# Kernel optimization log

Hardware: AMD Instinct MI355X
Metric: run time of the kernel (lower is better)

The kernel has to match this reference:

```python
import jax, jax.numpy as jnp
import numpy as np

N_NODES = 100000
NEG_SLOPE = 0.2  # PyG GATConv default


def gat_conv(x, W, att_src, att_dst, bias, src, dst, heads, out_ch, concat):
    """PyG-style GATConv (eval mode, self-loops already appended to src/dst).

    x: [N, F_in]; W: [F_in, heads*out_ch]; att_src/att_dst: [heads, out_ch];
    bias: [heads*out_ch] if concat else [out_ch].
    """
    n = x.shape[0]
    h = (x @ W).reshape(n, heads, out_ch)               # [N, H, C]
    a_s = jnp.einsum('nhc,hc->nh', h, att_src)          # [N, H]
    a_d = jnp.einsum('nhc,hc->nh', h, att_dst)          # [N, H]
    e = jax.nn.leaky_relu(a_s[src] + a_d[dst], NEG_SLOPE)  # [E, H]
    # segment softmax over incoming edges of each destination node
    m = jax.ops.segment_max(e, dst, num_segments=n)     # [N, H]
    ex = jnp.exp(e - m[dst])                            # [E, H]
    denom = jax.ops.segment_sum(ex, dst, num_segments=n)
    alpha = ex / denom[dst]                             # [E, H]
    msg = h[src] * alpha[:, :, None]                    # [E, H, C]
    out = jax.ops.segment_sum(msg, dst, num_segments=n) # [N, H, C]
    if concat:
        out = out.reshape(n, heads * out_ch)
    else:
        out = out.mean(axis=1)
    return out + bias


def setup_inputs() -> dict:
    key = jax.random.key(0)
    ks = jax.random.split(key, 12)
    N, F_IN, H1, C1, NC = N_NODES, 32, 8, 8, 2
    E = 3200000
    x = jax.random.normal(ks[0], (N, F_IN), dtype=jnp.float32)
    edge_index = jax.random.randint(ks[1], (2, E), 0, N, dtype=jnp.int64)
    s = 0.3
    return {
        'x': x,
        'edge_index': edge_index,
        'W1': jax.random.normal(ks[2], (F_IN, H1 * C1), dtype=jnp.float32) * s,
        'att_src1': jax.random.normal(ks[3], (H1, C1), dtype=jnp.float32) * s,
        'att_dst1': jax.random.normal(ks[4], (H1, C1), dtype=jnp.float32) * s,
        'b1': jnp.zeros((H1 * C1,), dtype=jnp.float32),
        'W2': jax.random.normal(ks[5], (H1 * C1, NC), dtype=jnp.float32) * s,
        'att_src2': jax.random.normal(ks[6], (1, NC), dtype=jnp.float32) * s,
        'att_dst2': jax.random.normal(ks[7], (1, NC), dtype=jnp.float32) * s,
        'b2': jnp.zeros((NC,), dtype=jnp.float32),
    }


def reference(x, W1, att_src1, att_dst1, b1, W2, att_src2, att_dst2, b2, edge_index):
    n = x.shape[0]
    # PyG GATConv adds self-loops by default
    loops = jnp.arange(n, dtype=edge_index.dtype)
    src = jnp.concatenate([edge_index[0], loops])
    dst = jnp.concatenate([edge_index[1], loops])
    # eval mode: all dropouts are identity
    h = jax.nn.elu(gat_conv(x, W1, att_src1, att_dst1, b1, src, dst, 8, 8, True))
    out = gat_conv(h, W2, att_src2, att_dst2, b2, src, dst, 1, 2, True)
    return jax.nn.log_softmax(out, axis=1)
```

## Files before the change

kernel.cpp:

```cpp
#include <hip/hip_runtime.h>
#include <math.h>

#define F_IN 32
#define NH 8
#define C1 8
#define D1 64
#define NEG 0.2f
#define LOG2E 1.44269504088896f
#define SHBIAS (-20.0f * LOG2E)

typedef int iv4 __attribute__((ext_vector_type(4)));
typedef unsigned short ushort_t;

__device__ __forceinline__ ushort_t f2bf(float f) {
    unsigned int b = __float_as_uint(f);
    return (ushort_t)((b + 0x7FFF + ((b >> 16) & 1)) >> 16);
}
__device__ __forceinline__ float bf2f(ushort_t u) {
    return __uint_as_float(((unsigned int)u) << 16);
}


__device__ __forceinline__ void node1_body(const float* __restrict__ x, const float* __restrict__ W1,
                                           const float* __restrict__ as1, const float* __restrict__ ad1,
                                           ushort_t* __restrict__ h1b, float* __restrict__ a_s,
                                           float* __restrict__ a_d, int N, int b) {
    __shared__ float sW[F_IN * D1];
    __shared__ float sA[2 * D1];
    for (int i = threadIdx.x; i < F_IN * D1; i += blockDim.x) sW[i] = W1[i];
    if (threadIdx.x < 2 * D1)
        sA[threadIdx.x] = (threadIdx.x < D1) ? as1[threadIdx.x] : ad1[threadIdx.x - D1];
    __syncthreads();
    int t = b * blockDim.x + threadIdx.x;
    int n = t >> 3, h = t & 7;
    if (n >= N) return;
    float xr[F_IN];
    const float4* xv = (const float4*)(x + n * F_IN);
#pragma unroll
    for (int k = 0; k < F_IN / 4; ++k) {
        float4 v = xv[k];
        xr[4 * k] = v.x; xr[4 * k + 1] = v.y; xr[4 * k + 2] = v.z; xr[4 * k + 3] = v.w;
    }
    float acc[C1];
#pragma unroll
    for (int c = 0; c < C1; ++c) acc[c] = 0.0f;
#pragma unroll
    for (int k = 0; k < F_IN; ++k) {
        float xk = xr[k];
#pragma unroll
        for (int c = 0; c < C1; ++c) acc[c] = fmaf(xk, sW[k * D1 + h * C1 + c], acc[c]);
    }
    float s_ = 0.0f, d_ = 0.0f;
    unsigned int w[4];
#pragma unroll
    for (int c = 0; c < C1; ++c) {
        s_ = fmaf(acc[c], sA[h * C1 + c], s_);
        d_ = fmaf(acc[c], sA[D1 + h * C1 + c], d_);
    }
#pragma unroll
    for (int k = 0; k < 4; ++k)
        w[k] = (unsigned int)f2bf(acc[2 * k]) | ((unsigned int)f2bf(acc[2 * k + 1]) << 16);
    iv4 wv = {(int)w[0], (int)w[1], (int)w[2], (int)w[3]};
    *(iv4*)(h1b + (size_t)n * D1 + h * C1) = wv;
    a_s[n * NH + h] = s_;
    a_d[n * NH + h] = d_;
}

__global__ void __launch_bounds__(256)
k_bhist_node1(const int* __restrict__ ei, int E4, int GA, int nbk,
              int* __restrict__ blkcnt,
              const float* __restrict__ x, const float* __restrict__ W1,
              const float* __restrict__ as1, const float* __restrict__ ad1,
              ushort_t* __restrict__ h1b, float* __restrict__ a_s, float* __restrict__ a_d,
              int N) {
    int g = blockIdx.x;
    if (g >= GA) { node1_body(x, W1, as1, ad1, h1b, a_s, a_d, N, g - GA); return; }
    __shared__ int hist[512];
    for (int i = threadIdx.x; i < nbk; i += 256) hist[i] = 0;
    __syncthreads();
    const iv4* d4 = (const iv4*)ei + E4;
    int base = g * 2048 + threadIdx.x;
#pragma unroll
    for (int k = 0; k < 8; ++k) {
        int idx = base + k * 256;
        if (idx < E4) {
            iv4 d = __builtin_nontemporal_load(d4 + idx);
            atomicAdd(&hist[d.x >> 8], 1);
            atomicAdd(&hist[d.y >> 8], 1);
            atomicAdd(&hist[d.z >> 8], 1);
            atomicAdd(&hist[d.w >> 8], 1);
        }
    }
    __syncthreads();
    for (int i = threadIdx.x; i < nbk; i += 256) blkcnt[(size_t)i * GA + g] = hist[i];
}

__global__ void k_scan_block(const int* __restrict__ in, int* __restrict__ tmp,
                             int* __restrict__ bsum, int F) {
    __shared__ int s[256];
    int i = blockIdx.x * 256 + threadIdx.x;
    int v = (i < F) ? in[i] : 0;
    s[threadIdx.x] = v;
    __syncthreads();
#pragma unroll
    for (int off = 1; off < 256; off <<= 1) {
        int t = (threadIdx.x >= off) ? s[threadIdx.x - off] : 0;
        __syncthreads();
        s[threadIdx.x] += t;
        __syncthreads();
    }
    tmp[i] = s[threadIdx.x] - v;
    if (threadIdx.x == 255) bsum[blockIdx.x] = s[255];
}

__global__ void k_scan_bsums1024(int* __restrict__ bsum, int nb) {
    __shared__ int s[1024];
    int t = threadIdx.x;
    s[t] = (t < nb) ? bsum[t] : 0;
    __syncthreads();
#pragma unroll
    for (int off = 1; off < 1024; off <<= 1) {
        int v = (t >= off) ? s[t - off] : 0;
        __syncthreads();
        s[t] += v;
        __syncthreads();
    }
    if (t < nb) bsum[t] = (t == 0) ? 0 : s[t - 1];
}

__global__ void k_scan_fin(const int* __restrict__ tmp, const int* __restrict__ bsum,
                           int* __restrict__ excl, int F, int E) {
    int i = blockIdx.x * blockDim.x + threadIdx.x;
    if (i > F) return;
    excl[i] = (i < F) ? (tmp[i] + bsum[i >> 8]) : E;
}

__global__ void __launch_bounds__(256)
k_part(const int* __restrict__ ei, int E4, int GA, int nbk,
       const int* __restrict__ excl, int* __restrict__ partbuf) {
    __shared__ int cur[512];
    int g = blockIdx.x;
    for (int i = threadIdx.x; i < nbk; i += 256) cur[i] = excl[(size_t)i * GA + g];
    __syncthreads();
    const iv4* s4 = (const iv4*)ei;
    const iv4* d4 = s4 + E4;
    int base = g * 2048 + threadIdx.x;
#pragma unroll
    for (int k = 0; k < 8; ++k) {
        int idx = base + k * 256;
        if (idx < E4) {
            iv4 d = __builtin_nontemporal_load(d4 + idx);
            iv4 s = __builtin_nontemporal_load(s4 + idx);
            int dd[4] = {d.x, d.y, d.z, d.w};
            int ss[4] = {s.x, s.y, s.z, s.w};
#pragma unroll
            for (int u = 0; u < 4; ++u) {
                int pos = atomicAdd(&cur[dd[u] >> 8], 1);
                partbuf[pos] = (ss[u] << 8) | (dd[u] & 255);
            }
        }
    }
}

__global__ void __launch_bounds__(256)
k_csr(const int* __restrict__ excl, const int* __restrict__ partbuf,
      int* __restrict__ ptr, int* __restrict__ srcs, int N, int GA, int nbk, int Et) {
    __shared__ int lcnt[256];
    __shared__ int lsc[256];
    int b = blockIdx.x;
    int tid = threadIdx.x;
    int pStart = excl[(size_t)b * GA];
    int pEnd   = excl[(size_t)(b + 1) * GA];
    int node = (b << 8) + tid;
    int exists = (node < N) ? 1 : 0;
    lcnt[tid] = exists;
    __syncthreads();
    for (int i = pStart + tid; i < pEnd; i += 256)
        atomicAdd(&lcnt[partbuf[i] & 255], 1);
    __syncthreads();
    int v = lcnt[tid];
    lsc[tid] = v;
    __syncthreads();
#pragma unroll
    for (int off = 1; off < 256; off <<= 1) {
        int t = (tid >= off) ? lsc[tid - off] : 0;
        __syncthreads();
        lsc[tid] += t;
        __syncthreads();
    }
    int exclv = lsc[tid] - v;
    int finalBase = pStart + (b << 8);
    if (exists) {
        int p = finalBase + exclv;
        ptr[node] = p;
        srcs[p] = node;
    }
    if (b == nbk - 1 && tid == 0) ptr[N] = Et;
    __syncthreads();
    lcnt[tid] = exclv + exists;
    __syncthreads();
    for (int i = pStart + tid; i < pEnd; i += 256) {
        int pv = partbuf[i];
        int r = atomicAdd(&lcnt[pv & 255], 1);
        srcs[finalBase + r] = pv >> 8;
    }
}


__device__ __forceinline__ float lrelu(float e) { return e > 0.0f ? e : NEG * e; }

__global__ void __launch_bounds__(256)
k_gat1(const int* __restrict__ ptr, const int* __restrict__ srcs,
       const float* __restrict__ a_s, const float* __restrict__ a_d,
       const ushort_t* __restrict__ h1b,
       const float* __restrict__ b1, const float* __restrict__ W2,
       const float* __restrict__ as2, const float* __restrict__ ad2,
       float* __restrict__ h2, float* __restrict__ a_s2o, float* __restrict__ a_d2o,
       int N) {
    int n = (blockIdx.x * blockDim.x + threadIdx.x) >> 6;
    if (n >= N) return;
    int l = threadIdx.x & 63;
    int j = l >> 3;
    int h = l & 7;
    int start = ptr[n], end = ptr[n + 1];
    float ad = a_d[n * NH + h];
    const ushort_t* hb = h1b + l;
    float den = 0.0f, acc = 0.0f;
    for (int base = start; base < end; base += 8) {
        int idxl = base + j;
        bool valid = idxl < end;
        if (!valid) idxl = end - 1;
        int s = srcs[idxl];
        float as = a_s[(s << 3) + h];
        float ex = exp2f(fmaf(lrelu(as + ad), LOG2E, SHBIAS));
        if (!valid) ex = 0.0f;
        den += ex;
        int s0 = __builtin_amdgcn_readlane(s, 0),  s1 = __builtin_amdgcn_readlane(s, 8);
        int s2 = __builtin_amdgcn_readlane(s, 16), s3 = __builtin_amdgcn_readlane(s, 24);
        int s4 = __builtin_amdgcn_readlane(s, 32), s5 = __builtin_amdgcn_readlane(s, 40);
        int s6 = __builtin_amdgcn_readlane(s, 48), s7 = __builtin_amdgcn_readlane(s, 56);
        float g0 = bf2f(hb[s0 << 6]), g1 = bf2f(hb[s1 << 6]);
        float g2 = bf2f(hb[s2 << 6]), g3 = bf2f(hb[s3 << 6]);
        float g4 = bf2f(hb[s4 << 6]), g5 = bf2f(hb[s5 << 6]);
        float g6 = bf2f(hb[s6 << 6]), g7 = bf2f(hb[s7 << 6]);
        int bl = l >> 3;
        float e0 = __shfl(ex, 0 + bl, 64),  e1 = __shfl(ex, 8 + bl, 64);
        float e2 = __shfl(ex, 16 + bl, 64), e3 = __shfl(ex, 24 + bl, 64);
        float e4 = __shfl(ex, 32 + bl, 64), e5 = __shfl(ex, 40 + bl, 64);
        float e6 = __shfl(ex, 48 + bl, 64), e7 = __shfl(ex, 56 + bl, 64);
        acc = fmaf(e0, g0, acc); acc = fmaf(e1, g1, acc);
        acc = fmaf(e2, g2, acc); acc = fmaf(e3, g3, acc);
        acc = fmaf(e4, g4, acc); acc = fmaf(e5, g5, acc);
        acc = fmaf(e6, g6, acc); acc = fmaf(e7, g7, acc);
    }
    den += __shfl_xor(den, 8, 64);
    den += __shfl_xor(den, 16, 64);
    den += __shfl_xor(den, 32, 64);
    den = __shfl(den, l >> 3, 64);
    float v = acc / den + b1[l];
    v = v > 0.0f ? v : expm1f(v);
    float r0 = v * W2[l * 2 + 0];
    float r1 = v * W2[l * 2 + 1];
#pragma unroll
    for (int off = 32; off; off >>= 1) {
        r0 += __shfl_xor(r0, off, 64);
        r1 += __shfl_xor(r1, off, 64);
    }
    if (l == 0) {
        h2[n * 2 + 0] = r0;
        h2[n * 2 + 1] = r1;
        a_s2o[n] = r0 * as2[0] + r1 * as2[1];
        a_d2o[n] = r0 * ad2[0] + r1 * ad2[1];
    }
}


__global__ void k_gat2(const int* __restrict__ ptr, const int* __restrict__ srcs,
                       const float* __restrict__ a_s2, const float* __restrict__ a_d2,
                       const float* __restrict__ h2, const float* __restrict__ b2,
                       float* __restrict__ out, int N) {
    int t = blockIdx.x * blockDim.x + threadIdx.x;
    int n = t >> 4;
    if (n >= N) return;
    int l = threadIdx.x & 15;
    int start = ptr[n], end = ptr[n + 1];
    float ad = a_d2[n];
    float den = 0.0f, a0 = 0.0f, a1 = 0.0f;
    for (int idx = start + l; idx < end; idx += 16) {
        int s = srcs[idx];
        float ex = exp2f(fmaf(lrelu(a_s2[s] + ad), LOG2E, SHBIAS));
        float2 hv = *(const float2*)(h2 + s * 2);
        den += ex;
        a0 = fmaf(ex, hv.x, a0);
        a1 = fmaf(ex, hv.y, a1);
    }
#pragma unroll
    for (int off = 8; off; off >>= 1) {
        den += __shfl_xor(den, off, 16);
        a0  += __shfl_xor(a0, off, 16);
        a1  += __shfl_xor(a1, off, 16);
    }
    if (l == 0) {
        float inv = 1.0f / den;
        float o0 = a0 * inv + b2[0];
        float o1 = a1 * inv + b2[1];
        float mx = fmaxf(o0, o1);
        float lse = mx + logf(__expf(o0 - mx) + __expf(o1 - mx));
        out[n * 2 + 0] = o0 - lse;
        out[n * 2 + 1] = o1 - lse;
    }
}

extern "C" void kernel_launch(void* const* d_in, const int* in_sizes, int n_in,
                              void* d_out, int out_size, void* d_ws, size_t ws_size,
                              hipStream_t stream) {
    const float* x   = (const float*)d_in[0];
    const int*   ei  = (const int*)d_in[1];
    const float* W1  = (const float*)d_in[2];
    const float* as1 = (const float*)d_in[3];
    const float* ad1 = (const float*)d_in[4];
    const float* b1  = (const float*)d_in[5];
    const float* W2  = (const float*)d_in[6];
    const float* as2 = (const float*)d_in[7];
    const float* ad2 = (const float*)d_in[8];
    const float* b2  = (const float*)d_in[9];
    float* out = (float*)d_out;

    const int N  = in_sizes[0] / F_IN;
    const int E  = in_sizes[1] / 2;
    const int E4 = E / 4;
    const int Et = E + N;
    const int nbk = (N + 255) >> 8;
    const int GA  = (E4 + 2047) >> 11;
    const int F   = nbk * GA;
    const int nbScan = (F + 255) >> 8;

    char* p = (char*)d_ws;
    ushort_t* h1b = (ushort_t*)p; p += (size_t)N * D1 * 2;
    float* a_s1 = (float*)p; p += (size_t)N * NH * 4;
    float* a_d1 = (float*)p; p += (size_t)N * NH * 4;
    float* h2   = (float*)p; p += (size_t)N * 2 * 4;
    float* a_s2 = (float*)p; p += (size_t)N * 4;
    float* a_d2 = (float*)p; p += (size_t)N * 4;
    int* blkcnt = (int*)p;   p += (size_t)F * 4;
    int* tmp    = (int*)p;   p += (size_t)nbScan * 256 * 4;
    int* bsum   = (int*)p;   p += (size_t)nbScan * 4;
    int* excl   = (int*)p;   p += (size_t)(F + 1) * 4;
    int* partbuf= (int*)p;   p += (size_t)E * 4;
    int* ptr    = (int*)p;   p += (size_t)(N + 1) * 4;
    int* srcs   = (int*)p;   p += (size_t)Et * 4;

    const int nN1 = (N * NH + 255) / 256;

    hipLaunchKernelGGL(k_bhist_node1, dim3(GA + nN1), dim3(256), 0, stream,
                       ei, E4, GA, nbk, blkcnt, x, W1, as1, ad1, h1b, a_s1, a_d1, N);

    hipLaunchKernelGGL(k_scan_block, dim3(nbScan), dim3(256), 0, stream, blkcnt, tmp, bsum, F);
    hipLaunchKernelGGL(k_scan_bsums1024, dim3(1), dim3(1024), 0, stream, bsum, nbScan);
    hipLaunchKernelGGL(k_scan_fin, dim3((F + 256) / 256), dim3(256), 0, stream,
                       tmp, bsum, excl, F, E);

    hipLaunchKernelGGL(k_part, dim3(GA), dim3(256), 0, stream, ei, E4, GA, nbk, excl, partbuf);

    hipLaunchKernelGGL(k_csr, dim3(nbk), dim3(256), 0, stream,
                       excl, partbuf, ptr, srcs, N, GA, nbk, Et);

    hipLaunchKernelGGL(k_gat1, dim3((N + 3) / 4), dim3(256), 0, stream,
                       ptr, srcs, a_s1, a_d1, h1b, b1, W2, as2, ad2, h2, a_s2, a_d2, N);

    hipLaunchKernelGGL(k_gat2, dim3((N * 16 + 255) / 256), dim3(256), 0, stream,
                       ptr, srcs, a_s2, a_d2, h2, b2, out, N);
}
```

Before: 218.3 us.

## Gather full head rows with 16-byte loads in GAT layer 1 and pack layer-2 node data

The layer-1 aggregation now has each lane load one 16-byte vector holding one head's 8 bf16 channels for its own edge. Previously each lane did eight scalar 2-byte gathers after readlane broadcasts and eight shuffles of the attention weights. Per-head partial sums are reduced across the eight edge slots with xor shuffles, and bias, ELU and the W2 projection are computed per lane from LDS-cached constants. Layer-2 inputs (a_s2, a_d2, h2) are packed into one float4 per node so each edge in k_gat2 needs a single 16-byte gather. In exchange, each lane holds eight accumulators, which adds register pressure and extra shuffle reductions at the end.

```diff
diff --git a/kernel.cpp b/kernel.cpp
--- a/kernel.cpp
+++ b/kernel.cpp
@@ -15,9 +15,6 @@
 __device__ __forceinline__ ushort_t f2bf(float f) {
     unsigned int b = __float_as_uint(f);
     return (ushort_t)((b + 0x7FFF + ((b >> 16) & 1)) >> 16);
-}
-__device__ __forceinline__ float bf2f(ushort_t u) {
-    return __uint_as_float(((unsigned int)u) << 16);
 }
 
 
@@ -215,8 +212,15 @@
        const ushort_t* __restrict__ h1b,
        const float* __restrict__ b1, const float* __restrict__ W2,
        const float* __restrict__ as2, const float* __restrict__ ad2,
-       float* __restrict__ h2, float* __restrict__ a_s2o, float* __restrict__ a_d2o,
-       int N) {
+       float4* __restrict__ p2, int N) {
+    __shared__ float sB1[D1];
+    __shared__ float sW2[D1 * 2];
+    __shared__ float sA2[4];
+    if (threadIdx.x < D1) sB1[threadIdx.x] = b1[threadIdx.x];
+    else if (threadIdx.x < D1 * 3) sW2[threadIdx.x - D1] = W2[threadIdx.x - D1];
+    else if (threadIdx.x < D1 * 3 + 2) sA2[threadIdx.x - D1 * 3] = as2[threadIdx.x - D1 * 3];
+    else if (threadIdx.x < D1 * 3 + 4) sA2[threadIdx.x - D1 * 3] = ad2[threadIdx.x - D1 * 3 - 2];
+    __syncthreads();
     int n = (blockIdx.x * blockDim.x + threadIdx.x) >> 6;
     if (n >= N) return;
     int l = threadIdx.x & 63;
@@ -224,8 +228,10 @@
     int h = l & 7;
     int start = ptr[n], end = ptr[n + 1];
     float ad = a_d[n * NH + h];
-    const ushort_t* hb = h1b + l;
-    float den = 0.0f, acc = 0.0f;
+    float den = 0.0f;
+    float acc[8];
+#pragma unroll
+    for (int c = 0; c < 8; ++c) acc[c] = 0.0f;
     for (int base = start; base < end; base += 8) {
         int idxl = base + j;
         bool valid = idxl < end;
@@ -235,64 +241,61 @@
         float ex = exp2f(fmaf(lrelu(as + ad), LOG2E, SHBIAS));
         if (!valid) ex = 0.0f;
         den += ex;
-        int s0 = __builtin_amdgcn_readlane(s, 0),  s1 = __builtin_amdgcn_readlane(s, 8);
-        int s2 = __builtin_amdgcn_readlane(s, 16), s3 = __builtin_amdgcn_readlane(s, 24);
-        int s4 = __builtin_amdgcn_readlane(s, 32), s5 = __builtin_amdgcn_readlane(s, 40);
-        int s6 = __builtin_amdgcn_readlane(s, 48), s7 = __builtin_amdgcn_readlane(s, 56);
-        float g0 = bf2f(hb[s0 << 6]), g1 = bf2f(hb[s1 << 6]);
-        float g2 = bf2f(hb[s2 << 6]), g3 = bf2f(hb[s3 << 6]);
-        float g4 = bf2f(hb[s4 << 6]), g5 = bf2f(hb[s5 << 6]);
-        float g6 = bf2f(hb[s6 << 6]), g7 = bf2f(hb[s7 << 6]);
-        int bl = l >> 3;
-        float e0 = __shfl(ex, 0 + bl, 64),  e1 = __shfl(ex, 8 + bl, 64);
-        float e2 = __shfl(ex, 16 + bl, 64), e3 = __shfl(ex, 24 + bl, 64);
-        float e4 = __shfl(ex, 32 + bl, 64), e5 = __shfl(ex, 40 + bl, 64);
-        float e6 = __shfl(ex, 48 + bl, 64), e7 = __shfl(ex, 56 + bl, 64);
-        acc = fmaf(e0, g0, acc); acc = fmaf(e1, g1, acc);
-        acc = fmaf(e2, g2, acc); acc = fmaf(e3, g3, acc);
-        acc = fmaf(e4, g4, acc); acc = fmaf(e5, g5, acc);
-        acc = fmaf(e6, g6, acc); acc = fmaf(e7, g7, acc);
+        iv4 hv = *(const iv4*)(h1b + ((size_t)s << 6) + (h << 3));
+        int dw[4] = {hv.x, hv.y, hv.z, hv.w};
+#pragma unroll
+        for (int k = 0; k < 4; ++k) {
+            float lo = __uint_as_float(((unsigned int)dw[k]) << 16);
+            float hi = __uint_as_float(((unsigned int)dw[k]) & 0xffff0000u);
+            acc[2 * k]     = fmaf(ex, lo, acc[2 * k]);
+            acc[2 * k + 1] = fmaf(ex, hi, acc[2 * k + 1]);
+        }
     }
     den += __shfl_xor(den, 8, 64);
     den += __shfl_xor(den, 16, 64);
     den += __shfl_xor(den, 32, 64);
-    den = __shfl(den, l >> 3, 64);
-    float v = acc / den + b1[l];
-    v = v > 0.0f ? v : expm1f(v);
-    float r0 = v * W2[l * 2 + 0];
-    float r1 = v * W2[l * 2 + 1];
-#pragma unroll
-    for (int off = 32; off; off >>= 1) {
-        r0 += __shfl_xor(r0, off, 64);
-        r1 += __shfl_xor(r1, off, 64);
-    }
+#pragma unroll
+    for (int c = 0; c < 8; ++c) {
+        acc[c] += __shfl_xor(acc[c], 8, 64);
+        acc[c] += __shfl_xor(acc[c], 16, 64);
+        acc[c] += __shfl_xor(acc[c], 32, 64);
+    }
+    float inv = 1.0f / den;
+    float r0 = 0.0f, r1 = 0.0f;
+#pragma unroll
+    for (int c = 0; c < 8; ++c) {
+        int col = (h << 3) + c;
+        float v = fmaf(acc[c], inv, sB1[col]);
+        v = v > 0.0f ? v : expm1f(v);
+        r0 = fmaf(v, sW2[col * 2 + 0], r0);
+        r1 = fmaf(v, sW2[col * 2 + 1], r1);
+    }
+    r0 += __shfl_xor(r0, 1, 64); r0 += __shfl_xor(r0, 2, 64); r0 += __shfl_xor(r0, 4, 64);
+    r1 += __shfl_xor(r1, 1, 64); r1 += __shfl_xor(r1, 2, 64); r1 += __shfl_xor(r1, 4, 64);
     if (l == 0) {
-        h2[n * 2 + 0] = r0;
-        h2[n * 2 + 1] = r1;
-        a_s2o[n] = r0 * as2[0] + r1 * as2[1];
-        a_d2o[n] = r0 * ad2[0] + r1 * ad2[1];
+        p2[n] = make_float4(r0 * sA2[0] + r1 * sA2[1],
+                            r0 * sA2[2] + r1 * sA2[3], r0, r1);
     }
 }
 
 
 __global__ void k_gat2(const int* __restrict__ ptr, const int* __restrict__ srcs,
-                       const float* __restrict__ a_s2, const float* __restrict__ a_d2,
-                       const float* __restrict__ h2, const float* __restrict__ b2,
+                       const float4* __restrict__ p2, const float* __restrict__ b2,
                        float* __restrict__ out, int N) {
     int t = blockIdx.x * blockDim.x + threadIdx.x;
     int n = t >> 4;
     if (n >= N) return;
     int l = threadIdx.x & 15;
     int start = ptr[n], end = ptr[n + 1];
-    float ad = a_d2[n];
+    float ad = p2[n].y;
     float den = 0.0f, a0 = 0.0f, a1 = 0.0f;
     for (int idx = start + l; idx < end; idx += 16) {
         int s = srcs[idx];
-        float ex = exp2f(fmaf(lrelu(a_s2[s] + ad), LOG2E, SHBIAS));
-        float2 hv = *(const float2*)(h2 + s * 2);
+        float4 ps = p2[s];
+        float ex = exp2f(fmaf(lrelu(ps.x + ad), LOG2E, SHBIAS));
         den += ex;
-        a0 = fmaf(ex, hv.x, a0);
-        a1 = fmaf(ex, hv.y, a1);
+        a0 = fmaf(ex, ps.z, a0);
+        a1 = fmaf(ex, ps.w, a1);
     }
 #pragma unroll
     for (int off = 8; off; off >>= 1) {
@@ -337,11 +340,9 @@
 
     char* p = (char*)d_ws;
     ushort_t* h1b = (ushort_t*)p; p += (size_t)N * D1 * 2;
+    float4* p2  = (float4*)p; p += (size_t)N * 16;
     float* a_s1 = (float*)p; p += (size_t)N * NH * 4;
     float* a_d1 = (float*)p; p += (size_t)N * NH * 4;
-    float* h2   = (float*)p; p += (size_t)N * 2 * 4;
-    float* a_s2 = (float*)p; p += (size_t)N * 4;
-    float* a_d2 = (float*)p; p += (size_t)N * 4;
     int* blkcnt = (int*)p;   p += (size_t)F * 4;
     int* tmp    = (int*)p;   p += (size_t)nbScan * 256 * 4;
     int* bsum   = (int*)p;   p += (size_t)nbScan * 4;
@@ -366,8 +367,8 @@
                        excl, partbuf, ptr, srcs, N, GA, nbk, Et);
 
     hipLaunchKernelGGL(k_gat1, dim3((N + 3) / 4), dim3(256), 0, stream,
-                       ptr, srcs, a_s1, a_d1, h1b, b1, W2, as2, ad2, h2, a_s2, a_d2, N);
+                       ptr, srcs, a_s1, a_d1, h1b, b1, W2, as2, ad2, p2, N);
 
     hipLaunchKernelGGL(k_gat2, dim3((N * 16 + 255) / 256), dim3(256), 0, stream,
-                       ptr, srcs, a_s2, a_d2, h2, b2, out, N);
-}
+                       ptr, srcs, p2, b2, out, N);
+}
```

Result: faster. 213.5 us (-2.2%).
